# Optimization experiments

Hardware: AMD Instinct MI355X
Metric: run time of the kernel (lower is better)

The kernel has to match this reference:

```python
import jax, jax.numpy as jnp
import numpy as np

ALPHA = 0.2  # LeakyReLU negative slope
NEG = -9e15


def _gat_heads(x, adj_mask, W, a):
    # x: (B,N,F); W: (H,F,O); a: (H,2O); adj_mask: (B,N,N) bool
    O = W.shape[-1]
    Wh = jnp.einsum('bnf,hfo->bhno', x, W)            # (B,H,N,O)
    e1 = jnp.einsum('bhno,ho->bhn', Wh, a[:, :O])     # Wh @ a[:O]
    e2 = jnp.einsum('bhno,ho->bhn', Wh, a[:, O:])     # Wh @ a[O:]
    e = jax.nn.leaky_relu(e1[:, :, :, None] + e2[:, :, None, :], ALPHA)  # (B,H,N,N)
    e = jnp.where(adj_mask[:, None], e, NEG)
    attn = jax.nn.softmax(e, axis=-1)
    return jnp.einsum('bhnm,bhmo->bhno', attn, Wh)    # (B,H,N,O)


def _gat_block(x, adj_mask, non_pad_mask, W_heads, a_heads, W_out, a_out):
    # multi-head layer, concat=True -> elu per head, then concat on feature dim
    h = jax.nn.elu(_gat_heads(x, adj_mask, W_heads, a_heads))  # (B,H,N,O)
    B, H, N, O = h.shape
    h = jnp.transpose(h, (0, 2, 1, 3)).reshape(B, N, H * O)
    h = h * non_pad_mask
    # out layer: single head, concat=False (no inner elu)
    h = _gat_heads(h, adj_mask, W_out[None], a_out[None])[:, 0]  # (B,N,noutput)
    h = h * non_pad_mask
    return jax.nn.elu(h)


def setup_inputs() -> dict:
    key = jax.random.key(0)
    ks = jax.random.split(key, 8)
    B, N = 32, 256
    vocab, F, O, H, OUT = 200, 300, 256, 8, 512
    fea = jax.random.randint(ks[0], (B, N), 0, vocab, dtype=jnp.int32)
    adj = jax.random.randint(ks[1], (B, N, N), 0, 2, dtype=jnp.int32)
    non_pad_mask = jnp.ones((B, N, 1), dtype=jnp.float32)
    embed = jax.random.normal(ks[2], (vocab, F), dtype=jnp.float32)
    W_heads = jax.random.normal(ks[3], (H, F, O), dtype=jnp.float32) / np.sqrt(F)
    a_heads = jax.random.normal(ks[4], (H, 2 * O), dtype=jnp.float32) / np.sqrt(2 * O)
    W_out = jax.random.normal(ks[5], (H * O, OUT), dtype=jnp.float32) / np.sqrt(H * O)
    a_out = jax.random.normal(ks[6], (2 * OUT,), dtype=jnp.float32) / np.sqrt(2 * OUT)
    return {"fea": fea, "adj": adj, "non_pad_mask": non_pad_mask, "embed": embed,
            "W_heads": W_heads, "a_heads": a_heads, "W_out": W_out, "a_out": a_out}


def reference(fea, adj, non_pad_mask, embed, W_heads, a_heads, W_out, a_out):
    adj_mask = adj > 0
    x = embed[fea]  # (B,N,F)
    # GAT_num = 1; dropout is identity in eval mode
    x = _gat_block(x, adj_mask, non_pad_mask, W_heads, a_heads, W_out, a_out)
    return x  # (B, N, 512)
```

## Files before the change

kernel.cpp:

```cpp
#include <hip/hip_runtime.h>
#include <math.h>


typedef _Float16 f16;
typedef __attribute__((ext_vector_type(8))) _Float16 f16x8;
typedef __attribute__((ext_vector_type(4))) _Float16 f16x4;
typedef __attribute__((ext_vector_type(4))) float f32x4;

__device__ __forceinline__ void async16(const void* g, void* lds) {
  __builtin_amdgcn_global_load_lds(
      (const __attribute__((address_space(1))) void*)g,
      (__attribute__((address_space(3))) void*)lds, 16, 0, 0);
}

__global__ __launch_bounds__(256) void k_prep(const int* __restrict__ fea,
                                              const float* __restrict__ embed,
                                              const float* __restrict__ Whd,
                                              const float* __restrict__ Wo,
                                              f16* __restrict__ x16,
                                              f16* __restrict__ WcT,
                                              f16* __restrict__ WoT,
                                              float* __restrict__ e_all) {
  int bid = blockIdx.x, tid = threadIdx.x;
  if (bid < 1280) {
    int idx = bid * 256 + tid;
    int row = idx / 40, c = idx % 40;
    int tok = fea[row];
    const float* eb = embed + (size_t)tok * 300;
    f16x8 v;
#pragma unroll
    for (int j = 0; j < 8; ++j) {
      int t = c * 8 + j;
      v[j] = (f16)((t < 300) ? eb[t] : 0.f);
    }
    *(f16x8*)&x16[(size_t)row * 320 + c * 8] = v;
  } else if (bid < 1920) {
    int r = bid - 1280;
    int zi = r * 256 + tid;
    if (zi < 16384) e_all[zi] = 0.f;
    __shared__ float tile[32][33];
    int bx = r % 10, q0 = r / 10;
    int by = q0 % 8, h = q0 / 8;
    int c = tid & 31, q = tid >> 5;
#pragma unroll
    for (int i = 0; i < 4; ++i) {
      int tt = q + i * 8;
      int t = bx * 32 + tt;
      float v = (t < 300) ? Whd[((size_t)h * 300 + t) * 256 + by * 32 + c] : 0.f;
      tile[tt][c] = v;
    }
    __syncthreads();
#pragma unroll
    for (int i = 0; i < 4; ++i) {
      int oo = q + i * 8;
      int gc = h * 256 + by * 32 + oo;
      WcT[(size_t)gc * 320 + bx * 32 + c] = (f16)tile[c][oo];
    }
  } else {
    int r = bid - 1920;
    __shared__ float tile[32][33];
    int bx = r % 64, by = r / 64;
    int c = tid & 31, q = tid >> 5;
#pragma unroll
    for (int i = 0; i < 4; ++i) {
      int kk = q + i * 8;
      tile[kk][c] = Wo[((size_t)bx * 32 + kk) * 512 + by * 32 + c];
    }
    __syncthreads();
#pragma unroll
    for (int i = 0; i < 4; ++i) {
      int oo = q + i * 8;
      WoT[((size_t)by * 32 + oo) * 2048 + bx * 32 + c] = (f16)tile[c][oo];
    }
  }
}

__global__ __launch_bounds__(512, 1) void k_l1(
    const f16* __restrict__ x16, const f16* __restrict__ WcT,
    const float* __restrict__ ah, const int* __restrict__ adj,
    const float* __restrict__ npm, f16* __restrict__ h1) {
  extern __shared__ __align__(16) char smem[];
  f16* AsB[2] = {(f16*)smem, (f16*)(smem + 65536)};
  f16* BsB[2] = {(f16*)(smem + 32768), (f16*)(smem + 98304)};
  char* WhB = smem;
  char* PB  = smem + 131072;
  float* e1f = (float*)(smem + 147456);
  float* e2f = (float*)(smem + 148480);

  const int bid = blockIdx.x;
  const int h = (bid >> 3) & 7;
  const int b = (bid & 7) * 4 + (bid >> 6);
  const int tid = threadIdx.x;
  const int wave = tid >> 6, lane = tid & 63;
  const int wm = wave >> 2, wn = wave & 3;
  const int lrow = lane & 15, quad = lane >> 4;
  const int srow = lane >> 3;
  const int scol = ((lane & 7) ^ (lane >> 3)) * 8;
  const int l7 = lrow & 7;

  if (tid < 256) e1f[tid] = 0.f;
  else e2f[tid - 256] = 0.f;

  f32x4 acc[8][4] = {};
  const f16* Ag = x16 + (size_t)b * 256 * 320;
  const f16* Bg = WcT + (size_t)h * 256 * 320;

#pragma unroll
  for (int j = 0; j < 4; ++j) {
    const int r0 = wave * 32 + j * 8;
    async16(Ag + (size_t)(r0 + srow) * 320 + scol, &AsB[0][r0 * 64]);
    async16(Bg + (size_t)(r0 + srow) * 320 + scol, &BsB[0][r0 * 64]);
  }
  __syncthreads();

#pragma unroll
  for (int t = 0; t < 5; ++t) {
    const f16* As = AsB[t & 1];
    const f16* Bs = BsB[t & 1];
    if (t < 4) {
      const int kn = (t + 1) * 64;
      f16* An = AsB[(t + 1) & 1];
      f16* Bn = BsB[(t + 1) & 1];
#pragma unroll
      for (int j = 0; j < 4; ++j) {
        const int r0 = wave * 32 + j * 8;
        async16(Ag + (size_t)(r0 + srow) * 320 + kn + scol, &An[r0 * 64]);
        async16(Bg + (size_t)(r0 + srow) * 320 + kn + scol, &Bn[r0 * 64]);
      }
    }
#pragma unroll
    for (int s = 0; s < 2; ++s) {
      const int sq = ((s * 4 + quad) ^ l7) * 8;
      f16x8 af[8], bf[4];
#pragma unroll
      for (int mt = 0; mt < 8; ++mt)
        af[mt] = *(const f16x8*)&As[(wm * 128 + mt * 16 + lrow) * 64 + sq];
#pragma unroll
      for (int nt = 0; nt < 4; ++nt)
        bf[nt] = *(const f16x8*)&Bs[(wn * 64 + nt * 16 + lrow) * 64 + sq];
#pragma unroll
      for (int mt = 0; mt < 8; ++mt)
#pragma unroll
        for (int nt = 0; nt < 4; ++nt)
          acc[mt][nt] = __builtin_amdgcn_mfma_f32_16x16x32_f16(af[mt], bf[nt], acc[mt][nt], 0, 0, 0);
    }
    __syncthreads();
  }

  const int* adjRow = adj + (size_t)b * 256 * 256;
  int4 ajR[4], ajN[4];
#pragma unroll
  for (int i = 0; i < 4; ++i)
    ajR[i] = *(const int4*)&adjRow[(size_t)(i * 8 + wave) * 256 + lane * 4];

  float a1v[4], a2v[4];
#pragma unroll
  for (int nt = 0; nt < 4; ++nt) {
    const int o = wn * 64 + nt * 16 + lrow;
    a1v[nt] = ah[h * 512 + o];
    a2v[nt] = ah[h * 512 + 256 + o];
  }
#pragma unroll
  for (int mt = 0; mt < 8; ++mt) {
    const int n0 = wm * 128 + mt * 16 + quad * 4;
    const int q16 = n0 >> 3;
    const int hoff = (n0 & 4) ? 8 : 0;
    float s1[4] = {0.f, 0.f, 0.f, 0.f}, s2[4] = {0.f, 0.f, 0.f, 0.f};
#pragma unroll
    for (int nt = 0; nt < 4; ++nt) {
      const int o = wn * 64 + nt * 16 + lrow;
      f16x4 v;
#pragma unroll
      for (int r = 0; r < 4; ++r) {
        v[r] = (f16)acc[mt][nt][r];
        s1[r] += acc[mt][nt][r] * a1v[nt];
        s2[r] += acc[mt][nt][r] * a2v[nt];
      }
      *(f16x4*)(WhB + o * 512 + ((q16 ^ (o & 7)) * 16 + hoff)) = v;
    }
#pragma unroll
    for (int r = 0; r < 4; ++r)
#pragma unroll
      for (int m = 1; m < 16; m <<= 1) {
        s1[r] += __shfl_xor(s1[r], m);
        s2[r] += __shfl_xor(s2[r], m);
      }
    if (lrow == 0) {
#pragma unroll
      for (int r = 0; r < 4; ++r) {
        atomicAdd(&e1f[n0 + r], s1[r]);
        atomicAdd(&e2f[n0 + r], s2[r]);
      }
    }
  }
  __syncthreads();

  float4 e2v = *(const float4*)&e2f[lane * 4];
  float e2m = fmaxf(fmaxf(e2v.x, e2v.y), fmaxf(e2v.z, e2v.w));
#pragma unroll
  for (int m = 1; m < 64; m <<= 1) e2m = fmaxf(e2m, __shfl_xor(e2m, m));

  for (int c = 0; c < 8; ++c) {
    if (c < 7) {
#pragma unroll
      for (int i = 0; i < 4; ++i)
        ajN[i] = *(const int4*)&adjRow[(size_t)((c + 1) * 32 + i * 8 + wave) * 256 + lane * 4];
    }
#pragma unroll
    for (int i = 0; i < 4; ++i) {
      int rl = i * 8 + wave;
      int n = c * 32 + rl;
      float er = e1f[n];
      float sh = er + e2m;
      sh = sh > 0.f ? sh : 0.2f * sh;
      int4 aj = ajR[i];
      float p0, p1, p2, p3;
      {
        float v = er + e2v.x; v = v > 0.f ? v : 0.2f * v;
        p0 = aj.x ? __expf(v - sh) : 0.f;
        v = er + e2v.y; v = v > 0.f ? v : 0.2f * v;
        p1 = aj.y ? __expf(v - sh) : 0.f;
        v = er + e2v.z; v = v > 0.f ? v : 0.2f * v;
        p2 = aj.z ? __expf(v - sh) : 0.f;
        v = er + e2v.w; v = v > 0.f ? v : 0.2f * v;
        p3 = aj.w ? __expf(v - sh) : 0.f;
      }
      float sm = p0 + p1 + p2 + p3;
#pragma unroll
      for (int m = 1; m < 64; m <<= 1) sm += __shfl_xor(sm, m);
      float rs = 1.f / sm;
      f16x4 pw;
      pw[0] = (f16)(p0 * rs); pw[1] = (f16)(p1 * rs);
      pw[2] = (f16)(p2 * rs); pw[3] = (f16)(p3 * rs);
      *(f16x4*)(PB + rl * 512 + (((lane >> 1) ^ (rl & 7)) * 16 + (lane & 1) * 8)) = pw;
    }
    __syncthreads();

    f32x4 acc2[2][2] = {};
#pragma unroll
    for (int kk = 0; kk < 8; ++kk) {
      f16x8 af2[2], bf2[2];
#pragma unroll
      for (int mtO = 0; mtO < 2; ++mtO) {
        int o = wave * 32 + mtO * 16 + lrow;
        af2[mtO] = *(const f16x8*)(WhB + o * 512 + (((kk * 4 + quad) ^ (o & 7)) * 16));
      }
#pragma unroll
      for (int ntN = 0; ntN < 2; ++ntN) {
        int rl = ntN * 16 + lrow;
        bf2[ntN] = *(const f16x8*)(PB + rl * 512 + (((kk * 4 + quad) ^ (rl & 7)) * 16));
      }
#pragma unroll
      for (int mtO = 0; mtO < 2; ++mtO)
#pragma unroll
        for (int ntN = 0; ntN < 2; ++ntN)
          acc2[mtO][ntN] = __builtin_amdgcn_mfma_f32_16x16x32_f16(af2[mtO], bf2[ntN], acc2[mtO][ntN], 0, 0, 0);
    }
    __syncthreads();

#pragma unroll
    for (int ntN = 0; ntN < 2; ++ntN) {
      int n = c * 32 + ntN * 16 + lrow;
      int gn = b * 256 + n;
      float pm = npm[gn];
#pragma unroll
      for (int mtO = 0; mtO < 2; ++mtO) {
        int o0 = wave * 32 + mtO * 16 + quad * 4;
        f16x4 st;
#pragma unroll
        for (int r = 0; r < 4; ++r) {
          float v = acc2[mtO][ntN][r];
          v = v > 0.f ? v : (__expf(v) - 1.f);
          st[r] = (f16)(v * pm);
        }
        *(f16x4*)&h1[(size_t)gn * 2048 + h * 256 + o0] = st;
      }
    }
#pragma unroll
    for (int i = 0; i < 4; ++i) ajR[i] = ajN[i];
  }
}

__global__ __launch_bounds__(256, 4) void k_gemm_sk(const f16* __restrict__ A,
                                                    const f16* __restrict__ BT,
                                                    f16* __restrict__ outSK,
                                                    const float* __restrict__ ao,
                                                    float* __restrict__ e12,
                                                    float* __restrict__ e22) {
  __shared__ f16 As[128 * 64];
  __shared__ f16 Bs[64 * 64];
  const int by = blockIdx.x, bx = blockIdx.y, kz = blockIdx.z;
  const int tid = threadIdx.x;
  const int wave = tid >> 6, lane = tid & 63;
  const int wm = wave >> 1, wn = wave & 1;
  const int lrow = lane & 15, quad = lane >> 4;
  const int srow = lane >> 3;
  const int scol = ((lane & 7) ^ (lane >> 3)) * 8;
  const int l7 = lrow & 7;

  f32x4 acc[4][2] = {};
  const f16* Ag = A + (size_t)by * 128 * 2048;
  const f16* Bg = BT + (size_t)bx * 64 * 2048;
  const int kbeg = kz * 1024;

  for (int k0 = kbeg; k0 < kbeg + 1024; k0 += 64) {
    __syncthreads();
#pragma unroll
    for (int j = 0; j < 4; ++j) {
      const int r0 = wave * 32 + j * 8;
      async16(Ag + (size_t)(r0 + srow) * 2048 + k0 + scol, &As[r0 * 64]);
    }
#pragma unroll
    for (int j = 0; j < 2; ++j) {
      const int r0 = wave * 16 + j * 8;
      async16(Bg + (size_t)(r0 + srow) * 2048 + k0 + scol, &Bs[r0 * 64]);
    }
    __syncthreads();
#pragma unroll
    for (int s = 0; s < 2; ++s) {
      const int sq = ((s * 4 + quad) ^ l7) * 8;
      f16x8 af[4], bf[2];
#pragma unroll
      for (int t = 0; t < 4; ++t)
        af[t] = *(const f16x8*)&As[(wm * 64 + t * 16 + lrow) * 64 + sq];
#pragma unroll
      for (int t = 0; t < 2; ++t)
        bf[t] = *(const f16x8*)&Bs[(wn * 32 + t * 16 + lrow) * 64 + sq];
#pragma unroll
      for (int mt = 0; mt < 4; ++mt)
#pragma unroll
        for (int nt = 0; nt < 2; ++nt)
          acc[mt][nt] = __builtin_amdgcn_mfma_f32_16x16x32_f16(af[mt], bf[nt], acc[mt][nt], 0, 0, 0);
    }
  }

  const int b = (by * 128) >> 8;
  const int nbase0 = (by * 128) & 255;
  f16* dst = outSK + (size_t)kz * 32 * 512 * 256;
#pragma unroll
  for (int mt = 0; mt < 4; ++mt) {
    const int nb = nbase0 + wm * 64 + mt * 16 + quad * 4;
#pragma unroll
    for (int nt = 0; nt < 2; ++nt) {
      const int gc = bx * 64 + wn * 32 + nt * 16 + lrow;
      f16x4 v;
#pragma unroll
      for (int r = 0; r < 4; ++r) v[r] = (f16)acc[mt][nt][r];
      *(f16x4*)&dst[((size_t)b * 512 + gc) * 256 + nb] = v;
    }
  }

  float a1v[2], a2v[2];
#pragma unroll
  for (int nt = 0; nt < 2; ++nt) {
    const int gc = bx * 64 + wn * 32 + nt * 16 + lrow;
    a1v[nt] = ao[gc];
    a2v[nt] = ao[512 + gc];
  }
#pragma unroll
  for (int mt = 0; mt < 4; ++mt) {
    float s1[4] = {0.f, 0.f, 0.f, 0.f}, s2[4] = {0.f, 0.f, 0.f, 0.f};
#pragma unroll
    for (int nt = 0; nt < 2; ++nt)
#pragma unroll
      for (int r = 0; r < 4; ++r) {
        s1[r] += acc[mt][nt][r] * a1v[nt];
        s2[r] += acc[mt][nt][r] * a2v[nt];
      }
#pragma unroll
    for (int r = 0; r < 4; ++r)
#pragma unroll
      for (int m = 1; m < 16; m <<= 1) {
        s1[r] += __shfl_xor(s1[r], m);
        s2[r] += __shfl_xor(s2[r], m);
      }
    if (lrow == 0) {
      const int nb = nbase0 + wm * 64 + mt * 16 + quad * 4;
#pragma unroll
      for (int r = 0; r < 4; ++r) {
        atomicAdd(&e12[b * 256 + nb + r], s1[r]);
        atomicAdd(&e22[b * 256 + nb + r], s2[r]);
      }
    }
  }
}

#define PSTRIDE 264

__global__ __launch_bounds__(256, 4) void k_attn2(
    const f16* __restrict__ sk, const float* __restrict__ e1g, const float* __restrict__ e2g,
    const int* __restrict__ adj, const float* __restrict__ npm, float* __restrict__ out) {
  int bid = blockIdx.x;
  int nt0 = (bid >> 3) & 3;
  int pair = (bid >> 5) * 8 + (bid & 7);
  int oh = pair >> 5, b = pair & 31;
  int n0 = nt0 * 64;
  __shared__ f16 P[64 * PSTRIDE];
  int tid = threadIdx.x;
  int wave = tid >> 6, lane = tid & 63;

  float4 e2v = *(const float4*)&e2g[b * 256 + lane * 4];
  float e2m = fmaxf(fmaxf(e2v.x, e2v.y), fmaxf(e2v.z, e2v.w));
#pragma unroll
  for (int m = 1; m < 64; m <<= 1) e2m = fmaxf(e2m, __shfl_xor(e2m, m));
#pragma unroll 4
  for (int i = 0; i < 16; ++i) {
    int row = i * 4 + wave;
    int gn = b * 256 + n0 + row;
    float er = e1g[b * 256 + n0 + row];
    float sh = er + e2m;
    sh = sh > 0.f ? sh : 0.2f * sh;
    int4 aj = *(const int4*)&adj[(size_t)gn * 256 + lane * 4];
    float p0, p1, p2, p3;
    {
      float v = er + e2v.x; v = v > 0.f ? v : 0.2f * v;
      p0 = aj.x ? __expf(v - sh) : 0.f;
      v = er + e2v.y; v = v > 0.f ? v : 0.2f * v;
      p1 = aj.y ? __expf(v - sh) : 0.f;
      v = er + e2v.z; v = v > 0.f ? v : 0.2f * v;
      p2 = aj.z ? __expf(v - sh) : 0.f;
      v = er + e2v.w; v = v > 0.f ? v : 0.2f * v;
      p3 = aj.w ? __expf(v - sh) : 0.f;
    }
    float sm = p0 + p1 + p2 + p3;
#pragma unroll
    for (int m = 1; m < 64; m <<= 1) sm += __shfl_xor(sm, m);
    float rs = 1.f / sm;
    f16x4 pw;
    pw[0] = (f16)(p0 * rs); pw[1] = (f16)(p1 * rs);
    pw[2] = (f16)(p2 * rs); pw[3] = (f16)(p3 * rs);
    *(f16x4*)&P[row * PSTRIDE + lane * 4] = pw;
  }
  __syncthreads();

  int lrow = lane & 15, quad = lane >> 4;
  f32x4 acc[2][4] = {};
  const f16* Ag0 = sk + ((size_t)b * 512 + oh * 128) * 256;
  const f16* Ag1 = Ag0 + (size_t)32 * 512 * 256;
#pragma unroll 2
  for (int k0 = 0; k0 < 256; k0 += 32) {
    f16x8 af[2], bf[4];
#pragma unroll
    for (int mt = 0; mt < 2; ++mt) {
      size_t off = (size_t)(wave * 32 + mt * 16 + lrow) * 256 + k0 + quad * 8;
      af[mt] = *(const f16x8*)&Ag0[off] + *(const f16x8*)&Ag1[off];
    }
#pragma unroll
    for (int nt = 0; nt < 4; ++nt)
      bf[nt] = *(const f16x8*)&P[(nt * 16 + lrow) * PSTRIDE + k0 + quad * 8];
#pragma unroll
    for (int mt = 0; mt < 2; ++mt)
#pragma unroll
      for (int nt = 0; nt < 4; ++nt)
        acc[mt][nt] = __builtin_amdgcn_mfma_f32_16x16x32_f16(af[mt], bf[nt], acc[mt][nt], 0, 0, 0);
  }
#pragma unroll
  for (int nt = 0; nt < 4; ++nt) {
    int nloc = nt * 16 + lrow;
    int gn = b * 256 + n0 + nloc;
    float pm = npm[gn];
#pragma unroll
    for (int mt = 0; mt < 2; ++mt) {
      int o0 = oh * 128 + wave * 32 + mt * 16 + quad * 4;
      float4 st;
      float v0 = acc[mt][nt][0] * pm;
      float v1 = acc[mt][nt][1] * pm;
      float v2 = acc[mt][nt][2] * pm;
      float v3 = acc[mt][nt][3] * pm;
      st.x = v0 > 0.f ? v0 : (__expf(v0) - 1.f);
      st.y = v1 > 0.f ? v1 : (__expf(v1) - 1.f);
      st.z = v2 > 0.f ? v2 : (__expf(v2) - 1.f);
      st.w = v3 > 0.f ? v3 : (__expf(v3) - 1.f);
      *(float4*)&out[(size_t)gn * 512 + o0] = st;
    }
  }
}

extern "C" void kernel_launch(void* const* d_in, const int* in_sizes, int n_in,
                              void* d_out, int out_size, void* d_ws, size_t ws_size,
                              hipStream_t stream) {
  (void)in_sizes; (void)n_in; (void)out_size; (void)ws_size;
  const int*   fea   = (const int*)d_in[0];
  const int*   adj   = (const int*)d_in[1];
  const float* npm   = (const float*)d_in[2];
  const float* embed = (const float*)d_in[3];
  const float* Whd   = (const float*)d_in[4];
  const float* ah    = (const float*)d_in[5];
  const float* Wo    = (const float*)d_in[6];
  const float* ao    = (const float*)d_in[7];
  float* out = (float*)d_out;

  char* ws = (char*)d_ws;
  f16* x16  = (f16*)ws;  ws += (size_t)8192 * 320 * 2;
  f16* WcT  = (f16*)ws;  ws += (size_t)2048 * 320 * 2;
  f16* WoT  = (f16*)ws;  ws += (size_t)512 * 2048 * 2;
  f16* h1   = (f16*)ws;  ws += (size_t)8192 * 2048 * 2;
  f16* Wh2sk = (f16*)ws; ws += (size_t)2 * 32 * 512 * 256 * 2;
  float* e12 = (float*)ws; ws += (size_t)8192 * 4;
  float* e22 = (float*)ws; ws += (size_t)8192 * 4;

  k_prep<<<2944, 256, 0, stream>>>(fea, embed, Whd, Wo, x16, WcT, WoT, e12);

  k_l1<<<256, 512, 149504, stream>>>(x16, WcT, ah, adj, npm, h1);

  k_gemm_sk<<<dim3(64, 8, 2), 256, 0, stream>>>(h1, WoT, Wh2sk, ao, e12, e22);
  k_attn2<<<512, 256, 0, stream>>>(Wh2sk, e12, e22, adj, npm, out);
}
```

Before: 184.5 us.

## Bit-pack adjacency once and restructure layer-1 attention into register-resident probabilities

The prep kernel now packs the int32 adjacency matrix into 64-bit ballot bitmasks once, and both attention stages read these masks instead of the full int32 rows, cutting adjacency traffic by 32x. In layer 1, the chunked loop that built probabilities in LDS and ran a sync-separated MFMA per 32 rows is replaced. Each wave now computes unnormalized probabilities for its own 32 rows straight into MFMA operand registers, applies the softmax normalization after accumulation, and drops the per-chunk barriers. The cost is an extra prep pass over adj and higher register pressure in k_l1. Probabilities are also rounded to fp16 before normalization, which slightly changes numerics.

```diff
diff --git a/kernel.cpp b/kernel.cpp
--- a/kernel.cpp
+++ b/kernel.cpp
@@ -6,6 +6,7 @@
 typedef __attribute__((ext_vector_type(8))) _Float16 f16x8;
 typedef __attribute__((ext_vector_type(4))) _Float16 f16x4;
 typedef __attribute__((ext_vector_type(4))) float f32x4;
+typedef unsigned long long u64;
 
 __device__ __forceinline__ void async16(const void* g, void* lds) {
   __builtin_amdgcn_global_load_lds(
@@ -17,10 +18,12 @@
                                               const float* __restrict__ embed,
                                               const float* __restrict__ Whd,
                                               const float* __restrict__ Wo,
+                                              const int* __restrict__ adj,
                                               f16* __restrict__ x16,
                                               f16* __restrict__ WcT,
                                               f16* __restrict__ WoT,
-                                              float* __restrict__ e_all) {
+                                              float* __restrict__ e_all,
+                                              u64* __restrict__ adjG) {
   int bid = blockIdx.x, tid = threadIdx.x;
   if (bid < 1280) {
     int idx = bid * 256 + tid;
@@ -56,7 +59,7 @@
       int gc = h * 256 + by * 32 + oo;
       WcT[(size_t)gc * 320 + bx * 32 + c] = (f16)tile[c][oo];
     }
-  } else {
+  } else if (bid < 2944) {
     int r = bid - 1920;
     __shared__ float tile[32][33];
     int bx = r % 64, by = r / 64;
@@ -72,20 +75,36 @@
       int oo = q + i * 8;
       WoT[((size_t)by * 32 + oo) * 2048 + bx * 32 + c] = (f16)tile[c][oo];
     }
+  } else {
+    int r = bid - 2944;
+    int wv = tid >> 6, ln = tid & 63;
+    int row = r * 64 + wv * 16;
+    const int* ar = adj + (size_t)row * 256;
+#pragma unroll 4
+    for (int i = 0; i < 16; ++i, ar += 256) {
+      u64 m0 = __ballot(ar[ln] != 0);
+      u64 m1 = __ballot(ar[64 + ln] != 0);
+      u64 m2 = __ballot(ar[128 + ln] != 0);
+      u64 m3 = __ballot(ar[192 + ln] != 0);
+      if (ln == 0) {
+        u64* d = &adjG[(size_t)(row + i) * 4];
+        d[0] = m0; d[1] = m1; d[2] = m2; d[3] = m3;
+      }
+    }
   }
 }
 
 __global__ __launch_bounds__(512, 1) void k_l1(
     const f16* __restrict__ x16, const f16* __restrict__ WcT,
-    const float* __restrict__ ah, const int* __restrict__ adj,
+    const float* __restrict__ ah, const u64* __restrict__ adjG,
     const float* __restrict__ npm, f16* __restrict__ h1) {
   extern __shared__ __align__(16) char smem[];
   f16* AsB[2] = {(f16*)smem, (f16*)(smem + 65536)};
   f16* BsB[2] = {(f16*)(smem + 32768), (f16*)(smem + 98304)};
   char* WhB = smem;
-  char* PB  = smem + 131072;
-  float* e1f = (float*)(smem + 147456);
-  float* e2f = (float*)(smem + 148480);
+  u64* adjB = (u64*)(smem + 131072);
+  float* e1f = (float*)(smem + 139264);
+  float* e2f = (float*)(smem + 140288);
 
   const int bid = blockIdx.x;
   const int h = (bid >> 3) & 7;
@@ -105,6 +124,7 @@
   const f16* Ag = x16 + (size_t)b * 256 * 320;
   const f16* Bg = WcT + (size_t)h * 256 * 320;
 
+  async16((const char*)adjG + (size_t)b * 8192 + tid * 16, (char*)adjB + tid * 16);
 #pragma unroll
   for (int j = 0; j < 4; ++j) {
     const int r0 = wave * 32 + j * 8;
@@ -147,12 +167,6 @@
     __syncthreads();
   }
 
-  const int* adjRow = adj + (size_t)b * 256 * 256;
-  int4 ajR[4], ajN[4];
-#pragma unroll
-  for (int i = 0; i < 4; ++i)
-    ajR[i] = *(const int4*)&adjRow[(size_t)(i * 8 + wave) * 256 + lane * 4];
-
   float a1v[4], a2v[4];
 #pragma unroll
   for (int nt = 0; nt < 4; ++nt) {
@@ -195,89 +209,77 @@
   }
   __syncthreads();
 
-  float4 e2v = *(const float4*)&e2f[lane * 4];
-  float e2m = fmaxf(fmaxf(e2v.x, e2v.y), fmaxf(e2v.z, e2v.w));
+  float4 e2q = *(const float4*)&e2f[lane * 4];
+  float e2m = fmaxf(fmaxf(e2q.x, e2q.y), fmaxf(e2q.z, e2q.w));
 #pragma unroll
   for (int m = 1; m < 64; m <<= 1) e2m = fmaxf(e2m, __shfl_xor(e2m, m));
 
-  for (int c = 0; c < 8; ++c) {
-    if (c < 7) {
-#pragma unroll
-      for (int i = 0; i < 4; ++i)
-        ajN[i] = *(const int4*)&adjRow[(size_t)((c + 1) * 32 + i * 8 + wave) * 256 + lane * 4];
-    }
-#pragma unroll
-    for (int i = 0; i < 4; ++i) {
-      int rl = i * 8 + wave;
-      int n = c * 32 + rl;
-      float er = e1f[n];
-      float sh = er + e2m;
-      sh = sh > 0.f ? sh : 0.2f * sh;
-      int4 aj = ajR[i];
-      float p0, p1, p2, p3;
-      {
-        float v = er + e2v.x; v = v > 0.f ? v : 0.2f * v;
-        p0 = aj.x ? __expf(v - sh) : 0.f;
-        v = er + e2v.y; v = v > 0.f ? v : 0.2f * v;
-        p1 = aj.y ? __expf(v - sh) : 0.f;
-        v = er + e2v.z; v = v > 0.f ? v : 0.2f * v;
-        p2 = aj.z ? __expf(v - sh) : 0.f;
-        v = er + e2v.w; v = v > 0.f ? v : 0.2f * v;
-        p3 = aj.w ? __expf(v - sh) : 0.f;
-      }
-      float sm = p0 + p1 + p2 + p3;
-#pragma unroll
-      for (int m = 1; m < 64; m <<= 1) sm += __shfl_xor(sm, m);
-      float rs = 1.f / sm;
-      f16x4 pw;
-      pw[0] = (f16)(p0 * rs); pw[1] = (f16)(p1 * rs);
-      pw[2] = (f16)(p2 * rs); pw[3] = (f16)(p3 * rs);
-      *(f16x4*)(PB + rl * 512 + (((lane >> 1) ^ (rl & 7)) * 16 + (lane & 1) * 8)) = pw;
-    }
-    __syncthreads();
-
-    f32x4 acc2[2][2] = {};
-#pragma unroll
-    for (int kk = 0; kk < 8; ++kk) {
-      f16x8 af2[2], bf2[2];
-#pragma unroll
-      for (int mtO = 0; mtO < 2; ++mtO) {
-        int o = wave * 32 + mtO * 16 + lrow;
-        af2[mtO] = *(const f16x8*)(WhB + o * 512 + (((kk * 4 + quad) ^ (o & 7)) * 16));
-      }
-#pragma unroll
-      for (int ntN = 0; ntN < 2; ++ntN) {
-        int rl = ntN * 16 + lrow;
-        bf2[ntN] = *(const f16x8*)(PB + rl * 512 + (((kk * 4 + quad) ^ (rl & 7)) * 16));
-      }
-#pragma unroll
-      for (int mtO = 0; mtO < 2; ++mtO)
-#pragma unroll
-        for (int ntN = 0; ntN < 2; ++ntN)
-          acc2[mtO][ntN] = __builtin_amdgcn_mfma_f32_16x16x32_f16(af2[mtO], bf2[ntN], acc2[mtO][ntN], 0, 0, 0);
-    }
-    __syncthreads();
-
-#pragma unroll
-    for (int ntN = 0; ntN < 2; ++ntN) {
-      int n = c * 32 + ntN * 16 + lrow;
-      int gn = b * 256 + n;
-      float pm = npm[gn];
-#pragma unroll
-      for (int mtO = 0; mtO < 2; ++mtO) {
-        int o0 = wave * 32 + mtO * 16 + quad * 4;
-        f16x4 st;
-#pragma unroll
-        for (int r = 0; r < 4; ++r) {
-          float v = acc2[mtO][ntN][r];
-          v = v > 0.f ? v : (__expf(v) - 1.f);
-          st[r] = (f16)(v * pm);
-        }
-        *(f16x4*)&h1[(size_t)gn * 2048 + h * 256 + o0] = st;
-      }
-    }
-#pragma unroll
-    for (int i = 0; i < 4; ++i) ajR[i] = ajN[i];
+  const int nb0 = wave * 32;
+  const float er0 = e1f[nb0 + lrow];
+  const float er1 = e1f[nb0 + 16 + lrow];
+  float sh0 = er0 + e2m; sh0 = sh0 > 0.f ? sh0 : 0.2f * sh0;
+  float sh1 = er1 + e2m; sh1 = sh1 > 0.f ? sh1 : 0.2f * sh1;
+  u64 aw0[4], aw1[4];
+#pragma unroll
+  for (int q = 0; q < 4; ++q) {
+    aw0[q] = adjB[(nb0 + lrow) * 4 + q];
+    aw1[q] = adjB[(nb0 + 16 + lrow) * 4 + q];
+  }
+
+  f16x8 p0[8], p1[8];
+  float ss0 = 0.f, ss1 = 0.f;
+#pragma unroll
+  for (int k0 = 0; k0 < 8; ++k0) {
+    const float* e2p = &e2f[k0 * 32 + quad * 8];
+    float4 ea = *(const float4*)e2p;
+    float4 eb = *(const float4*)(e2p + 4);
+    unsigned int b0 = (unsigned int)(aw0[k0 >> 1] >> ((k0 & 1) * 32 + quad * 8)) & 0xFFu;
+    unsigned int b1 = (unsigned int)(aw1[k0 >> 1] >> ((k0 & 1) * 32 + quad * 8)) & 0xFFu;
+    float e2arr[8] = {ea.x, ea.y, ea.z, ea.w, eb.x, eb.y, eb.z, eb.w};
+    f16x8 q0, q1;
+#pragma unroll
+    for (int j = 0; j < 8; ++j) {
+      float v = er0 + e2arr[j]; v = v > 0.f ? v : 0.2f * v;
+      float p = (b0 >> j) & 1 ? __expf(v - sh0) : 0.f;
+      ss0 += p; q0[j] = (f16)p;
+      v = er1 + e2arr[j]; v = v > 0.f ? v : 0.2f * v;
+      p = (b1 >> j) & 1 ? __expf(v - sh1) : 0.f;
+      ss1 += p; q1[j] = (f16)p;
+    }
+    p0[k0] = q0; p1[k0] = q1;
+  }
+  ss0 += __shfl_xor(ss0, 16); ss0 += __shfl_xor(ss0, 32);
+  ss1 += __shfl_xor(ss1, 16); ss1 += __shfl_xor(ss1, 32);
+  const float rs0 = 1.f / ss0, rs1 = 1.f / ss1;
+  const float pm0 = npm[b * 256 + nb0 + lrow];
+  const float pm1 = npm[b * 256 + nb0 + 16 + lrow];
+  f16* h1b0 = &h1[(size_t)(b * 256 + nb0 + lrow) * 2048 + h * 256];
+  f16* h1b1 = &h1[(size_t)(b * 256 + nb0 + 16 + lrow) * 2048 + h * 256];
+  const char* wp = WhB + (size_t)lrow * 512;
+
+#pragma unroll 4
+  for (int of = 0; of < 16; ++of) {
+    f32x4 c0 = {}, c1 = {};
+    const char* wo = wp + of * 8192;
+#pragma unroll
+    for (int k0 = 0; k0 < 8; ++k0) {
+      f16x8 af = *(const f16x8*)(wo + (((k0 * 4 + quad) ^ l7) * 16));
+      c0 = __builtin_amdgcn_mfma_f32_16x16x32_f16(af, p0[k0], c0, 0, 0, 0);
+      c1 = __builtin_amdgcn_mfma_f32_16x16x32_f16(af, p1[k0], c1, 0, 0, 0);
+    }
+    const int o0 = of * 16 + quad * 4;
+    f16x4 s0, s1;
+#pragma unroll
+    for (int r = 0; r < 4; ++r) {
+      float v = c0[r] * rs0;
+      v = v > 0.f ? v : (__expf(v) - 1.f);
+      s0[r] = (f16)(v * pm0);
+      v = c1[r] * rs1;
+      v = v > 0.f ? v : (__expf(v) - 1.f);
+      s1[r] = (f16)(v * pm1);
+    }
+    *(f16x4*)(h1b0 + o0) = s0;
+    *(f16x4*)(h1b1 + o0) = s1;
   }
 }
 
@@ -389,7 +391,7 @@
 
 __global__ __launch_bounds__(256, 4) void k_attn2(
     const f16* __restrict__ sk, const float* __restrict__ e1g, const float* __restrict__ e2g,
-    const int* __restrict__ adj, const float* __restrict__ npm, float* __restrict__ out) {
+    const u64* __restrict__ adjG, const float* __restrict__ npm, float* __restrict__ out) {
   int bid = blockIdx.x;
   int nt0 = (bid >> 3) & 3;
   int pair = (bid >> 5) * 8 + (bid & 7);
@@ -410,17 +412,18 @@
     float er = e1g[b * 256 + n0 + row];
     float sh = er + e2m;
     sh = sh > 0.f ? sh : 0.2f * sh;
-    int4 aj = *(const int4*)&adj[(size_t)gn * 256 + lane * 4];
+    u64 word = adjG[(size_t)gn * 4 + (lane >> 4)];
+    unsigned int bits = (unsigned int)(word >> ((lane & 15) * 4)) & 0xFu;
     float p0, p1, p2, p3;
     {
       float v = er + e2v.x; v = v > 0.f ? v : 0.2f * v;
-      p0 = aj.x ? __expf(v - sh) : 0.f;
+      p0 = bits & 1 ? __expf(v - sh) : 0.f;
       v = er + e2v.y; v = v > 0.f ? v : 0.2f * v;
-      p1 = aj.y ? __expf(v - sh) : 0.f;
+      p1 = bits & 2 ? __expf(v - sh) : 0.f;
       v = er + e2v.z; v = v > 0.f ? v : 0.2f * v;
-      p2 = aj.z ? __expf(v - sh) : 0.f;
+      p2 = bits & 4 ? __expf(v - sh) : 0.f;
       v = er + e2v.w; v = v > 0.f ? v : 0.2f * v;
-      p3 = aj.w ? __expf(v - sh) : 0.f;
+      p3 = bits & 8 ? __expf(v - sh) : 0.f;
     }
     float sm = p0 + p1 + p2 + p3;
 #pragma unroll
@@ -498,11 +501,12 @@
   f16* Wh2sk = (f16*)ws; ws += (size_t)2 * 32 * 512 * 256 * 2;
   float* e12 = (float*)ws; ws += (size_t)8192 * 4;
   float* e22 = (float*)ws; ws += (size_t)8192 * 4;
-
-  k_prep<<<2944, 256, 0, stream>>>(fea, embed, Whd, Wo, x16, WcT, WoT, e12);
-
-  k_l1<<<256, 512, 149504, stream>>>(x16, WcT, ah, adj, npm, h1);
+  u64* adjG = (u64*)ws;  ws += (size_t)8192 * 4 * 8;
+
+  k_prep<<<3072, 256, 0, stream>>>(fea, embed, Whd, Wo, adj, x16, WcT, WoT, e12, adjG);
+
+  k_l1<<<256, 512, 141312, stream>>>(x16, WcT, ah, adjG, npm, h1);
 
   k_gemm_sk<<<dim3(64, 8, 2), 256, 0, stream>>>(h1, WoT, Wh2sk, ao, e12, e22);
-  k_attn2<<<512, 256, 0, stream>>>(Wh2sk, e12, e22, adj, npm, out);
+  k_attn2<<<512, 256, 0, stream>>>(Wh2sk, e12, e22, adjG, npm, out);
 }
```

Result: no change. 183.5 us (-0.5%).
